# Kernel tuning notes

Measured on AMD Instinct MI355X. Metric: run time of the kernel, lower is better.

## Reference

```python
import jax, jax.numpy as jnp
import numpy as np

B, S, H = 4, 8192, 768
E, K = 8, 2


def setup_inputs() -> dict:
    key = jax.random.key(0)
    ks = jax.random.split(key, 5)
    scale = 1.0 / np.sqrt(H)
    x = jax.random.normal(ks[0], (B, S, H), dtype=jnp.float32)
    router_w = jax.random.uniform(ks[1], (E, H), jnp.float32, -scale, scale)   # torch Linear(h, E).weight
    router_b = jax.random.uniform(ks[2], (E,), jnp.float32, -scale, scale)
    expert_w = jax.random.uniform(ks[3], (E, H, H), jnp.float32, -scale, scale)  # [E, out, in]
    expert_b = jax.random.uniform(ks[4], (E, H), jnp.float32, -scale, scale)
    return {"x": x, "router_w": router_w, "router_b": router_b,
            "expert_w": expert_w, "expert_b": expert_b}


def reference(x, router_w, router_b, expert_w, expert_b):
    # Router: scores [b,s,E] -> softmax -> top-k probs/ids
    scores = jnp.einsum('bsh,eh->bse', x, router_w) + router_b
    probs = jax.nn.softmax(scores, axis=-1)
    top_probs, expert_ids = jax.lax.top_k(probs, K)          # [b,s,K]
    # Dense grouped expert linears: y[b,s,e,d] = x[b,s,:] @ W_e.T + b_e
    y = jnp.einsum('bsh,edh->bsed', x, expert_w) + expert_b   # [b,s,E,H]
    # Gather the k selected experts' outputs per token
    out_k = jnp.take_along_axis(y, expert_ids[..., None], axis=2)  # [b,s,K,H]
    # Normalize top-k probs and combine
    w = top_probs / (jnp.sum(top_probs, axis=-1, keepdims=True) + 1e-9)  # [b,s,K]
    out = jnp.einsum('bsk,bskh->bsh', w, out_k)
    return out
```

## Files before the change

### kernel.cpp

```cpp
#include <hip/hip_runtime.h>
#include <stdint.h>

#define TOK 32768
#define H 768
#define NE 8
#define CAP 8192
#define BM 128
#define BN 128
#define BK 32

typedef __bf16 bf16x8 __attribute__((ext_vector_type(8)));
typedef float  f32x4  __attribute__((ext_vector_type(4)));

#define OFF_ASSIGN 256
#define OFF_L0 (OFF_ASSIGN + TOK*16)
#define OFF_W0 (OFF_L0 + NE*CAP*4)
#define OFF_L1 (OFF_W0 + NE*CAP*4)
#define OFF_W1 (OFF_L1 + NE*CAP*4)
#define OFF_XB (OFF_W1 + NE*CAP*4)
#define OFF_WB (OFF_XB + (size_t)TOK*H*2)

__device__ __forceinline__ unsigned short f2bf(float f) {
    uint32_t u = __builtin_bit_cast(uint32_t, f);
    u = (u + 0x7fffu + ((u >> 16) & 1u)) >> 16;
    return (unsigned short)u;
}

__device__ __forceinline__ void async_cp16(const void* g, void* l) {
    __builtin_amdgcn_global_load_lds(
        (const __attribute__((address_space(1))) void*)g,
        (__attribute__((address_space(3))) void*)l, 16, 0, 0);
}

__global__ __launch_bounds__(256) void convert_w(const float* __restrict__ src,
                                                 unsigned short* __restrict__ dst, int n4) {
    int i = blockIdx.x * 256 + threadIdx.x;
    if (i < n4) {
        float4 v = ((const float4*)src)[i];
        ushort4 h;
        h.x = f2bf(v.x); h.y = f2bf(v.y); h.z = f2bf(v.z); h.w = f2bf(v.w);
        ((ushort4*)dst)[i] = h;
    }
}

__global__ __launch_bounds__(256) void router_kernel(
    const float* __restrict__ x, const float* __restrict__ rw, const float* __restrict__ rb,
    unsigned short* __restrict__ xb, int4* __restrict__ assign)
{
    int wid  = threadIdx.x >> 6;
    int lane = threadIdx.x & 63;
    int token = blockIdx.x * 4 + wid;

    const float4* xr  = (const float4*)(x + (size_t)token * H);
    const float4* rw4 = (const float4*)rw;

    float s[NE];
    #pragma unroll
    for (int e = 0; e < NE; e++) s[e] = 0.f;

    #pragma unroll
    for (int i = 0; i < 3; i++) {
        int p = lane + 64 * i;
        float4 xv = xr[p];
        ushort4 xh;
        xh.x = f2bf(xv.x); xh.y = f2bf(xv.y); xh.z = f2bf(xv.z); xh.w = f2bf(xv.w);
        ((ushort4*)(xb + (size_t)token * H))[p] = xh;
        #pragma unroll
        for (int e = 0; e < NE; e++) {
            float4 wv = rw4[e * 192 + p];
            s[e] += xv.x * wv.x + xv.y * wv.y + xv.z * wv.z + xv.w * wv.w;
        }
    }
    #pragma unroll
    for (int e = 0; e < NE; e++) {
        float v = s[e];
        #pragma unroll
        for (int off = 32; off; off >>= 1) v += __shfl_xor(v, off, 64);
        s[e] = v + rb[e];
    }
    if (lane == 0) {
        int e0 = 0;
        #pragma unroll
        for (int e = 1; e < NE; e++) if (s[e] > s[e0]) e0 = e;
        int e1 = -1;
        #pragma unroll
        for (int e = 0; e < NE; e++) {
            if (e == e0) continue;
            if (e1 < 0 || s[e] > s[e1]) e1 = e;
        }
        float mx = s[e0];
        float Z = 0.f;
        #pragma unroll
        for (int e = 0; e < NE; e++) Z += __expf(s[e] - mx);
        float p0 = __expf(s[e0] - mx) / Z;
        float p1 = __expf(s[e1] - mx) / Z;
        float inv = 1.f / (p0 + p1 + 1e-9f);
        int4 a;
        a.x = e0; a.y = e1;
        a.z = __float_as_int(p0 * inv);
        a.w = __float_as_int(p1 * inv);
        assign[token] = a;
    }
}

#define SCAT_T 1024
__global__ __launch_bounds__(256) void scatter_kernel(
    const int4* __restrict__ assign, int* __restrict__ counts,
    int* __restrict__ l0, float* __restrict__ w0,
    int* __restrict__ l1, float* __restrict__ w1)
{
    __shared__ int lcnt[2 * NE];
    __shared__ int lbase[2 * NE];
    int tid = threadIdx.x;
    if (tid < 2 * NE) lcnt[tid] = 0;
    __syncthreads();

    int4 a[SCAT_T / 256];
    int  r0[SCAT_T / 256], r1[SCAT_T / 256];
    #pragma unroll
    for (int j = 0; j < SCAT_T / 256; j++) {
        int token = blockIdx.x * SCAT_T + j * 256 + tid;
        a[j] = assign[token];
        r0[j] = atomicAdd(&lcnt[a[j].x], 1);
        r1[j] = atomicAdd(&lcnt[NE + a[j].y], 1);
    }
    __syncthreads();
    if (tid < 2 * NE) lbase[tid] = atomicAdd(&counts[tid], lcnt[tid]);
    __syncthreads();

    #pragma unroll
    for (int j = 0; j < SCAT_T / 256; j++) {
        int token = blockIdx.x * SCAT_T + j * 256 + tid;
        int p0 = lbase[a[j].x] + r0[j];
        int p1 = lbase[NE + a[j].y] + r1[j];
        l0[a[j].x * CAP + p0] = token; w0[a[j].x * CAP + p0] = __int_as_float(a[j].z);
        l1[a[j].y * CAP + p1] = token; w1[a[j].y * CAP + p1] = __int_as_float(a[j].w);
    }
}

template <bool ACCUM>
__global__ __launch_bounds__(256) void expert_gemm(
    const unsigned short* __restrict__ xb, const unsigned short* __restrict__ wb,
    const float* __restrict__ eb, const int* __restrict__ counts,
    const int* __restrict__ lists, const float* __restrict__ wlists,
    float* __restrict__ out)
{
    int e   = blockIdx.z;
    int cnt = counts[e];
    int m0  = blockIdx.x * BM;
    if (m0 >= cnt) return;
    int n0  = blockIdx.y * BN;

    __shared__ unsigned short As[BM][BK];
    __shared__ unsigned short Bs[BN][BK];
    __shared__ int   toks[BM];
    __shared__ float wts[BM];

    int tid = threadIdx.x;
    if (tid < BM) {
        int g = m0 + tid;
        int t = 0; float w = 0.f;
        if (g < cnt) { t = lists[e * CAP + g]; w = wlists[e * CAP + g]; }
        toks[tid] = t; wts[tid] = w;
    }
    __syncthreads();

    int wid = tid >> 6, lane = tid & 63;
    int wm = wid & 1, wn = wid >> 1;
    int quad = lane >> 4, r16 = lane & 15;

    int srow = wid * 16 + (lane >> 2);
    int c8   = (lane & 3) * 8;
    int rA0 = srow, rA1 = 64 + srow;

    const unsigned short* srcA0 = xb + (size_t)toks[rA0] * H + c8;
    const unsigned short* srcA1 = xb + (size_t)toks[rA1] * H + c8;
    const unsigned short* srcB0 = wb + ((size_t)e * H + n0 + rA0) * H + c8;
    const unsigned short* srcB1 = wb + ((size_t)e * H + n0 + rA1) * H + c8;
    char* dstA0 = (char*)&As[0][0] + wid * 1024;
    char* dstA1 = dstA0 + 4096;
    char* dstB0 = (char*)&Bs[0][0] + wid * 1024;
    char* dstB1 = dstB0 + 4096;

    f32x4 acc[4][4] = {};

    for (int k0 = 0; k0 < H; k0 += BK) {
        async_cp16(srcA0 + k0, dstA0);
        async_cp16(srcA1 + k0, dstA1);
        async_cp16(srcB0 + k0, dstB0);
        async_cp16(srcB1 + k0, dstB1);
        __syncthreads();

        bf16x8 a[4], b[4];
        #pragma unroll
        for (int mi = 0; mi < 4; mi++)
            a[mi] = *(const bf16x8*)&As[wm * 64 + mi * 16 + r16][quad * 8];
        #pragma unroll
        for (int ni = 0; ni < 4; ni++)
            b[ni] = *(const bf16x8*)&Bs[wn * 64 + ni * 16 + r16][quad * 8];

        #pragma unroll
        for (int mi = 0; mi < 4; mi++)
            #pragma unroll
            for (int ni = 0; ni < 4; ni++)
                acc[mi][ni] = __builtin_amdgcn_mfma_f32_16x16x32_bf16(a[mi], b[ni], acc[mi][ni], 0, 0, 0);
        __syncthreads();
    }

    float bias[4];
    #pragma unroll
    for (int ni = 0; ni < 4; ni++)
        bias[ni] = eb[e * H + n0 + wn * 64 + ni * 16 + r16];

    #pragma unroll
    for (int mi = 0; mi < 4; mi++) {
        int rowb = wm * 64 + mi * 16 + quad * 4;
        #pragma unroll
        for (int r = 0; r < 4; r++) {
            int row = rowb + r;
            if (m0 + row < cnt) {
                float w = wts[row];
                float* orow = out + (size_t)toks[row] * H + n0 + wn * 64;
                #pragma unroll
                for (int ni = 0; ni < 4; ni++) {
                    float v = (acc[mi][ni][r] + bias[ni]) * w;
                    if (ACCUM) v += orow[ni * 16 + r16];
                    orow[ni * 16 + r16] = v;
                }
            }
        }
    }
}

extern "C" void kernel_launch(void* const* d_in, const int* in_sizes, int n_in,
                              void* d_out, int out_size, void* d_ws, size_t ws_size,
                              hipStream_t stream) {
    const float* x   = (const float*)d_in[0];
    const float* rw  = (const float*)d_in[1];
    const float* rb  = (const float*)d_in[2];
    const float* ew  = (const float*)d_in[3];
    const float* ebv = (const float*)d_in[4];
    float* out = (float*)d_out;

    char* ws = (char*)d_ws;
    int*   counts = (int*)ws;
    int4*  assign = (int4*)(ws + OFF_ASSIGN);
    int*   l0     = (int*)(ws + OFF_L0);
    float* w0     = (float*)(ws + OFF_W0);
    int*   l1     = (int*)(ws + OFF_L1);
    float* w1     = (float*)(ws + OFF_W1);
    unsigned short* xb = (unsigned short*)(ws + OFF_XB);
    unsigned short* wb = (unsigned short*)(ws + OFF_WB);

    hipMemsetAsync(counts, 0, 64, stream);

    int n4 = NE * H * H / 4;
    convert_w<<<(n4 + 255) / 256, 256, 0, stream>>>(ew, wb, n4);
    router_kernel<<<TOK / 4, 256, 0, stream>>>(x, rw, rb, xb, assign);
    scatter_kernel<<<TOK / SCAT_T, 256, 0, stream>>>(assign, counts, l0, w0, l1, w1);

    dim3 grid(CAP / BM, H / BN, NE);
    expert_gemm<false><<<grid, 256, 0, stream>>>(xb, wb, ebv, counts,      l0, w0, out);
    expert_gemm<true ><<<grid, 256, 0, stream>>>(xb, wb, ebv, counts + NE, l1, w1, out);
}
```

Baseline: 367.4 us.

## Double-buffer expert GEMM LDS tiles and XOR-swizzle columns

Measured after the change: 377.5 us. 2.7% more time.

```diff
diff --git a/kernel.cpp b/kernel.cpp
--- a/kernel.cpp
+++ b/kernel.cpp
@@ -8,6 +8,7 @@
 #define BM 128
 #define BN 128
 #define BK 32
+#define KITERS (H / BK)
 
 typedef __bf16 bf16x8 __attribute__((ext_vector_type(8)));
 typedef float  f32x4  __attribute__((ext_vector_type(4)));
@@ -151,8 +152,8 @@
     if (m0 >= cnt) return;
     int n0  = blockIdx.y * BN;
 
-    __shared__ unsigned short As[BM][BK];
-    __shared__ unsigned short Bs[BN][BK];
+    __shared__ unsigned short As[2][BM][BK];
+    __shared__ unsigned short Bs[2][BM][BK];
     __shared__ int   toks[BM];
     __shared__ float wts[BM];
 
@@ -170,41 +171,52 @@
     int quad = lane >> 4, r16 = lane & 15;
 
     int srow = wid * 16 + (lane >> 2);
-    int c8   = (lane & 3) * 8;
+    int cswE = (((lane & 3) ^ ((srow >> 1) & 3)) * 8);
     int rA0 = srow, rA1 = 64 + srow;
 
-    const unsigned short* srcA0 = xb + (size_t)toks[rA0] * H + c8;
-    const unsigned short* srcA1 = xb + (size_t)toks[rA1] * H + c8;
-    const unsigned short* srcB0 = wb + ((size_t)e * H + n0 + rA0) * H + c8;
-    const unsigned short* srcB1 = wb + ((size_t)e * H + n0 + rA1) * H + c8;
-    char* dstA0 = (char*)&As[0][0] + wid * 1024;
-    char* dstA1 = dstA0 + 4096;
-    char* dstB0 = (char*)&Bs[0][0] + wid * 1024;
-    char* dstB1 = dstB0 + 4096;
+    const unsigned short* srcA0 = xb + (size_t)toks[rA0] * H + cswE;
+    const unsigned short* srcA1 = xb + (size_t)toks[rA1] * H + cswE;
+    const unsigned short* srcB0 = wb + ((size_t)e * H + n0 + rA0) * H + cswE;
+    const unsigned short* srcB1 = wb + ((size_t)e * H + n0 + rA1) * H + cswE;
+    char* dA = (char*)&As[0][0][0] + wid * 1024;
+    char* dB = (char*)&Bs[0][0][0] + wid * 1024;
+
+    int csel = (quad ^ ((r16 >> 1) & 3)) * 8;
 
     f32x4 acc[4][4] = {};
 
-    for (int k0 = 0; k0 < H; k0 += BK) {
-        async_cp16(srcA0 + k0, dstA0);
-        async_cp16(srcA1 + k0, dstA1);
-        async_cp16(srcB0 + k0, dstB0);
-        async_cp16(srcB1 + k0, dstB1);
+    async_cp16(srcA0, dA);
+    async_cp16(srcA1, dA + 4096);
+    async_cp16(srcB0, dB);
+    async_cp16(srcB1, dB + 4096);
+
+    for (int k = 0; k < KITERS; k++) {
+        int buf = k & 1;
         __syncthreads();
 
+        if (k + 1 < KITERS) {
+            int koff = (k + 1) * BK;
+            char* nA = dA + (1 - buf) * 8192;
+            char* nB = dB + (1 - buf) * 8192;
+            async_cp16(srcA0 + koff, nA);
+            async_cp16(srcA1 + koff, nA + 4096);
+            async_cp16(srcB0 + koff, nB);
+            async_cp16(srcB1 + koff, nB + 4096);
+        }
+
         bf16x8 a[4], b[4];
         #pragma unroll
         for (int mi = 0; mi < 4; mi++)
-            a[mi] = *(const bf16x8*)&As[wm * 64 + mi * 16 + r16][quad * 8];
+            a[mi] = *(const bf16x8*)&As[buf][wm * 64 + mi * 16 + r16][csel];
         #pragma unroll
         for (int ni = 0; ni < 4; ni++)
-            b[ni] = *(const bf16x8*)&Bs[wn * 64 + ni * 16 + r16][quad * 8];
+            b[ni] = *(const bf16x8*)&Bs[buf][wn * 64 + ni * 16 + r16][csel];
 
         #pragma unroll
         for (int mi = 0; mi < 4; mi++)
             #pragma unroll
             for (int ni = 0; ni < 4; ni++)
                 acc[mi][ni] = __builtin_amdgcn_mfma_f32_16x16x32_bf16(a[mi], b[ni], acc[mi][ni], 0, 0, 0);
-        __syncthreads();
     }
 
     float bias[4];
```
